# Kernel tuning notes

Hardware: AMD Instinct MI355X
Metric: run time of the kernel (lower is better)

Reference implementation:

```python
import jax, jax.numpy as jnp
import numpy as np

TEMP = 0.07
BASE_TEMP = 0.07
LOSS_WEIGHT = 0.5
BN_EPS = 1e-5

N, C_IN, H, W = 8, 512, 128, 128
FEAT_DIM = 256
N_ANCHOR, N_VIEW = 152, 26  # total_classes, n_view from max_samples=4096


def _embed(x, W1, b1, gamma, beta, W2, b2):
    # x: [N, C, H, W]; 1x1 conv -> BatchNorm (batch stats, training mode) -> ReLU -> 1x1 conv -> L2 norm over channel
    h = jnp.einsum('nchw,dc->ndhw', x, W1) + b1[None, :, None, None]
    mu = h.mean(axis=(0, 2, 3), keepdims=True)
    var = h.var(axis=(0, 2, 3), keepdims=True)
    h = (h - mu) * jax.lax.rsqrt(var + BN_EPS)
    h = h * gamma[None, :, None, None] + beta[None, :, None, None]
    h = jax.nn.relu(h)
    z = jnp.einsum('nchw,dc->ndhw', h, W2) + b2[None, :, None, None]
    nrm = jnp.sqrt(jnp.sum(z * z, axis=1, keepdims=True))
    return z / jnp.maximum(nrm, 1e-12)


def _contrastive(fS, fT, labels):
    # fS, fT: [A, V, d]; labels: [A]
    A, V, d = fS.shape
    anchor = jnp.transpose(fS, (1, 0, 2)).reshape(V * A, d)  # cat(unbind(dim=1))
    contrast = jax.lax.stop_gradient(jnp.transpose(fT, (1, 0, 2)).reshape(V * A, d))
    logits = (anchor @ contrast.T) / TEMP  # [M, M]
    logits = logits - jax.lax.stop_gradient(logits.max(axis=1, keepdims=True))
    base = (labels[:, None] == labels[None, :]).astype(logits.dtype)  # [A, A]
    mask = jnp.tile(base, (V, V))  # repeat(anchor_count, contrast_count)
    neg_mask = 1.0 - mask
    M = V * A
    mask = mask * (1.0 - jnp.eye(M, dtype=logits.dtype))  # remove self-pairs
    exp_l = jnp.exp(logits)
    neg = (exp_l * neg_mask).sum(axis=1, keepdims=True)
    log_prob = logits - jnp.log(exp_l + neg)
    mean_log_prob_pos = (mask * log_prob).sum(axis=1) / (mask.sum(axis=1) + 1e-6)
    return (-(TEMP / BASE_TEMP) * mean_log_prob_pos).mean()


def setup_inputs() -> dict:
    key = jax.random.key(0)
    ks = jax.random.split(key, 16)
    inp = {
        'preds_S': jax.random.normal(ks[0], (N, C_IN, H, W), jnp.float32),
        'preds_T': jax.random.normal(ks[1], (N, C_IN, H, W), jnp.float32),
        'sample_batch': jax.random.randint(ks[2], (N_ANCHOR,), 0, N, jnp.int32),
        'sample_idx': jax.random.randint(ks[3], (N_ANCHOR, N_VIEW), 0, H * W, jnp.int32),
        'labels_': jax.random.randint(ks[4], (N_ANCHOR,), 0, 19, jnp.int32),
    }
    def conv_params(k, cin, cout):
        k1, k2 = jax.random.split(k)
        return (jax.random.normal(k1, (cout, cin), jnp.float32) * 0.02,
                jnp.zeros((cout,), jnp.float32))
    for pfx, kw, kb in (('s', ks[5], ks[6]), ('t', ks[7], ks[8])):
        W1, b1 = conv_params(kw, C_IN, C_IN)
        W2, b2 = conv_params(kb, C_IN, FEAT_DIM)
        inp[f'{pfx}_W1'], inp[f'{pfx}_b1'] = W1, b1
        inp[f'{pfx}_gamma'] = jnp.ones((C_IN,), jnp.float32)
        inp[f'{pfx}_beta'] = jnp.zeros((C_IN,), jnp.float32)
        inp[f'{pfx}_W2'], inp[f'{pfx}_b2'] = W2, b2
    return inp


def reference(preds_S, preds_T, sample_batch, sample_idx, labels_,
              s_W1, s_b1, s_gamma, s_beta, s_W2, s_b2,
              t_W1, t_b1, t_gamma, t_beta, t_W2, t_b2):
    zS = _embed(preds_S, s_W1, s_b1, s_gamma, s_beta, s_W2, s_b2)
    zT = _embed(preds_T, t_W1, t_b1, t_gamma, t_beta, t_W2, t_b2)
    n, d, h, w = zS.shape
    fS = jnp.transpose(zS, (0, 2, 3, 1)).reshape(n, h * w, d)
    fT = jnp.transpose(zT, (0, 2, 3, 1)).reshape(n, h * w, d)
    # hard-anchor gather: [A, V, d]
    fS_ = fS[sample_batch[:, None], sample_idx]
    fT_ = fT[sample_batch[:, None], sample_idx]
    loss = _contrastive(fS_, fT_, labels_) + _contrastive(fT_, fS_, labels_)
    return LOSS_WEIGHT * loss
```

## Files before the change

kernel.cpp:

```cpp
#include <hip/hip_runtime.h>
#include <hip/hip_bf16.h>

#define A_N 152
#define V_N 26
#define M_N 3952
#define M_PAD 3968
#define CIN 512
#define FDIM 256
#define HW_SZ 16384
#define P_TOT 131072.0f
#define TEMP_INV 14.285714285714286f
#define NGRP 2048
#define LCAP 64

typedef __attribute__((ext_vector_type(8))) short bf16x8;
typedef __attribute__((ext_vector_type(4))) float f32x4;

static __device__ __forceinline__ short f2bf(float x){
  union { float f; unsigned u; } v; v.f = x;
  unsigned r = (v.u + 0x7FFFu + ((v.u >> 16) & 1u)) >> 16;
  return (short)r;
}

static __device__ __forceinline__ bf16x8 ldfrag(const short* __restrict__ base, int ld,
                                                int row, int k, int lane){
  return *(const bf16x8*)(base + (size_t)(row + (lane & 15)) * ld + k + ((lane >> 4) << 3));
}

static __device__ __forceinline__ bf16x8 ldfragP(const short* __restrict__ base,
                                                 int dtile, int ktile, int lane){
  return *(const bf16x8*)(base + ((((size_t)dtile << 4) + ktile) << 9) + (lane << 3));
}

static __device__ __forceinline__ void cvt4(short* __restrict__ lds, float4 v,
                                            int px, int tid){
  lds[(px+0)*512 + (tid ^ (((px+0)&7)<<3))] = f2bf(v.x);
  lds[(px+1)*512 + (tid ^ (((px+1)&7)<<3))] = f2bf(v.y);
  lds[(px+2)*512 + (tid ^ (((px+2)&7)<<3))] = f2bf(v.z);
  lds[(px+3)*512 + (tid ^ (((px+3)&7)<<3))] = f2bf(v.w);
}

__global__ void castw_kernel(const float* __restrict__ a0, short* __restrict__ o0,
                             const float* __restrict__ a1, short* __restrict__ o1,
                             const float* __restrict__ a2, short* __restrict__ o2,
                             const float* __restrict__ a3, short* __restrict__ o3){
  const float* a; short* o; int n;
  switch (blockIdx.y){
    case 0: a = a0; o = o0; n = CIN*CIN; break;
    case 1: a = a1; o = o1; n = CIN*CIN; break;
    case 2: a = a2; o = o2; n = FDIM*CIN; break;
    default: a = a3; o = o3; n = FDIM*CIN; break;
  }
  int i = blockIdx.x * 256 + threadIdx.x;
  if (i >= n) return;
  if (blockIdx.y < 2){
    int j  = i & 7;
    int ln = (i >> 3) & 63;
    int kt = (i >> 9) & 15;
    int dt = i >> 13;
    int row = dt * 16 + (ln & 15);
    int col = kt * 32 + ((ln >> 4) << 3) + j;
    o[i] = f2bf(a[row * CIN + col]);
  } else {
    o[i] = f2bf(a[i]);
  }
}

__global__ __launch_bounds__(64) void build_lists_kernel(
    const int* __restrict__ sb, const int* __restrict__ si,
    int* __restrict__ counts, int* __restrict__ lists){
  int m = blockIdx.x * 64 + threadIdx.x;
  if (m >= M_N) return;
  int a = m % A_N, v = m / A_N;
  int pix = si[a * V_N + v];
  int g = sb[a] * 256 + (pix >> 6);
  int slot = atomicAdd(&counts[g], 1);
  if (slot < LCAP) lists[g * LCAP + slot] = m | ((pix & 63) << 16);
}

__global__ __launch_bounds__(512, 2) void stats_kernel(
    const float* __restrict__ xS, const float* __restrict__ xT,
    const short* __restrict__ w1S, const short* __restrict__ w1T,
    float* __restrict__ stats,
    const int* __restrict__ counts, const int* __restrict__ lists,
    short* __restrict__ xsS, short* __restrict__ xsT){
  __shared__ short lds[128 * 512];
  const int t = blockIdx.y;
  const float* __restrict__ x = t ? xT : xS;
  const short* __restrict__ w1 = t ? w1T : w1S;
  float* sums = stats + t * 1024;
  short* __restrict__ xs = t ? xsT : xsS;

  const int tid  = threadIdx.x;
  const int lane = tid & 63;
  const int wave = tid >> 6;

  float rs[4] = {0.f,0.f,0.f,0.f};
  float rq[4] = {0.f,0.f,0.f,0.f};

  for (int it = 0; it < 4; ++it){
    const int T   = blockIdx.x + it * 256;
    const int n   = T >> 7;
    const int hw0 = (T & 127) << 7;
    const float* src = x + ((size_t)(n * CIN + tid)) * HW_SZ + hw0;

    const int g0 = T * 2, g1 = g0 + 1;
    int cnt0 = counts[g0]; if (cnt0 > LCAP) cnt0 = LCAP;
    int cnt1 = counts[g1]; if (cnt1 > LCAP) cnt1 = LCAP;

    #pragma unroll
    for (int ch = 0; ch < 8; ++ch){
      float4 v0 = *(const float4*)(src + ch * 16 +  0);
      float4 v1 = *(const float4*)(src + ch * 16 +  4);
      float4 v2 = *(const float4*)(src + ch * 16 +  8);
      float4 v3 = *(const float4*)(src + ch * 16 + 12);
      cvt4(lds, v0, ch * 16 +  0, tid);
      cvt4(lds, v1, ch * 16 +  4, tid);
      cvt4(lds, v2, ch * 16 +  8, tid);
      cvt4(lds, v3, ch * 16 + 12, tid);
    }
    __syncthreads();

    f32x4 acc[8][4] = {};
    {
      bf16x8 c0 = ldfragP(w1, wave*4 + 0, 0, lane);
      bf16x8 c1 = ldfragP(w1, wave*4 + 1, 0, lane);
      bf16x8 c2 = ldfragP(w1, wave*4 + 2, 0, lane);
      bf16x8 c3 = ldfragP(w1, wave*4 + 3, 0, lane);
      for (int kt = 0; kt < 16; ++kt){
        const int kn = (kt + 1) & 15;
        bf16x8 n0 = ldfragP(w1, wave*4 + 0, kn, lane);
        bf16x8 n1 = ldfragP(w1, wave*4 + 1, kn, lane);
        bf16x8 n2 = ldfragP(w1, wave*4 + 2, kn, lane);
        bf16x8 n3 = ldfragP(w1, wave*4 + 3, kn, lane);
        const int kk = kt << 5;
        #pragma unroll
        for (int pi = 0; pi < 8; ++pi){
          int px = pi*16 + (lane & 15);
          int c  = (kk + ((lane >> 4) << 3)) ^ ((px & 7) << 3);
          bf16x8 af = *(const bf16x8*)(lds + px*512 + c);
          acc[pi][0] = __builtin_amdgcn_mfma_f32_16x16x32_bf16(af, c0, acc[pi][0], 0, 0, 0);
          acc[pi][1] = __builtin_amdgcn_mfma_f32_16x16x32_bf16(af, c1, acc[pi][1], 0, 0, 0);
          acc[pi][2] = __builtin_amdgcn_mfma_f32_16x16x32_bf16(af, c2, acc[pi][2], 0, 0, 0);
          acc[pi][3] = __builtin_amdgcn_mfma_f32_16x16x32_bf16(af, c3, acc[pi][3], 0, 0, 0);
        }
        c0 = n0; c1 = n1; c2 = n2; c3 = n3;
      }
    }
    #pragma unroll
    for (int di = 0; di < 4; ++di){
      float s = 0.f, q2 = 0.f;
      #pragma unroll
      for (int pi = 0; pi < 8; ++pi)
        #pragma unroll
        for (int r = 0; r < 4; ++r){ float vv = acc[pi][di][r]; s += vv; q2 += vv*vv; }
      rs[di] += s; rq[di] += q2;
    }

    for (int s = 0; s < cnt0; ++s){
      int e = lists[g0 * LCAP + s];
      int m = e & 0xFFFF, px = e >> 16;
      xs[(size_t)m * CIN + tid] = lds[px * 512 + (tid ^ ((px & 7) << 3))];
    }
    for (int s = 0; s < cnt1; ++s){
      int e = lists[g1 * LCAP + s];
      int m = e & 0xFFFF, px = (e >> 16) + 64;
      xs[(size_t)m * CIN + tid] = lds[px * 512 + (tid ^ ((px & 7) << 3))];
    }
    __syncthreads();
  }
  #pragma unroll
  for (int di = 0; di < 4; ++di){
    float s = rs[di], q2 = rq[di];
    s  += __shfl_xor(s, 16, 64);  s  += __shfl_xor(s, 32, 64);
    q2 += __shfl_xor(q2, 16, 64); q2 += __shfl_xor(q2, 32, 64);
    if ((lane & 48) == 0){
      int d = wave * 64 + di*16 + lane;
      atomicAdd(&sums[d], s);
      atomicAdd(&sums[512 + d], q2);
    }
  }
}

__global__ __launch_bounds__(256) void conv1_kernel(
    const short* __restrict__ xsS, const short* __restrict__ xsT,
    const short* __restrict__ w1S, const short* __restrict__ w1T,
    const float* __restrict__ stats,
    const float* __restrict__ gS, const float* __restrict__ bS,
    const float* __restrict__ gT, const float* __restrict__ bT,
    short* __restrict__ hrS, short* __restrict__ hrT){
  const int t = blockIdx.z;
  const short* xs = t ? xsT : xsS;
  const short* w1 = t ? w1T : w1S;
  const float* sums  = stats + t * 1024;
  const float* gamma = t ? gT : gS;
  const float* beta  = t ? bT : bS;
  short* hr = t ? hrT : hrS;

  const int lane = threadIdx.x & 63;
  const int wave = threadIdx.x >> 6;
  const int m0 = blockIdx.x * 16;
  const int dt0 = (blockIdx.y * 4 + wave) * 4;
  const int d0  = dt0 * 16;

  f32x4 acc[4] = {};
  for (int kk = 0; kk < CIN; kk += 32){
    bf16x8 a = ldfrag(xs, CIN, m0, kk, lane);
    #pragma unroll
    for (int di = 0; di < 4; ++di){
      bf16x8 b = ldfragP(w1, dt0 + di, kk >> 5, lane);
      acc[di] = __builtin_amdgcn_mfma_f32_16x16x32_bf16(a, b, acc[di], 0, 0, 0);
    }
  }
  const float invP = 1.f / P_TOT;
  #pragma unroll
  for (int di = 0; di < 4; ++di){
    int d = d0 + di*16 + (lane & 15);
    float mu  = sums[d] * invP;
    float var = sums[512 + d] * invP - mu * mu;
    float sc  = gamma[d] * rsqrtf(var + 1e-5f);
    float sh  = beta[d] - mu * sc;
    #pragma unroll
    for (int r = 0; r < 4; ++r){
      int m = m0 + ((lane >> 4) << 2) + r;
      float v = fmaxf(acc[di][r] * sc + sh, 0.f);
      hr[(size_t)m * CIN + d] = f2bf(v);
    }
  }
}

__global__ __launch_bounds__(256) void conv2_kernel(
    const short* __restrict__ hrS, const short* __restrict__ hrT,
    const short* __restrict__ w2S, const short* __restrict__ w2T,
    const float* __restrict__ b2S, const float* __restrict__ b2T,
    short* __restrict__ fS, short* __restrict__ fT){
  __shared__ float ssum[4][16];
  const int t = blockIdx.y;
  const short* hr = t ? hrT : hrS;
  const short* w2 = t ? w2T : w2S;
  const float* b2 = t ? b2T : b2S;
  short* f = t ? fT : fS;

  const int lane = threadIdx.x & 63;
  const int wave = threadIdx.x >> 6;
  const int m0 = blockIdx.x * 16;
  const int e0 = wave * 64;

  f32x4 acc[4] = {};
  for (int kk = 0; kk < CIN; kk += 32){
    bf16x8 a = ldfrag(hr, CIN, m0, kk, lane);
    #pragma unroll
    for (int ei = 0; ei < 4; ++ei){
      bf16x8 b = ldfrag(w2, CIN, e0 + ei*16, kk, lane);
      acc[ei] = __builtin_amdgcn_mfma_f32_16x16x32_bf16(a, b, acc[ei], 0, 0, 0);
    }
  }
  float z[4][4];
  float part[4] = {0.f,0.f,0.f,0.f};
  #pragma unroll
  for (int ei = 0; ei < 4; ++ei){
    int e = e0 + ei*16 + (lane & 15);
    float bb = b2[e];
    #pragma unroll
    for (int r = 0; r < 4; ++r){
      float v = acc[ei][r] + bb;
      z[ei][r] = v;
      part[r] += v * v;
    }
  }
  #pragma unroll
  for (int r = 0; r < 4; ++r){
    float p = part[r];
    p += __shfl_xor(p, 1, 64); p += __shfl_xor(p, 2, 64);
    p += __shfl_xor(p, 4, 64); p += __shfl_xor(p, 8, 64);
    part[r] = p;
  }
  if ((lane & 15) == 0){
    #pragma unroll
    for (int r = 0; r < 4; ++r) ssum[wave][((lane >> 4) << 2) + r] = part[r];
  }
  __syncthreads();
  #pragma unroll
  for (int r = 0; r < 4; ++r){
    int mrow = ((lane >> 4) << 2) + r;
    float tot = ssum[0][mrow] + ssum[1][mrow] + ssum[2][mrow] + ssum[3][mrow];
    float sc = 1.f / fmaxf(sqrtf(tot), 1e-12f);
    #pragma unroll
    for (int ei = 0; ei < 4; ++ei){
      int e = e0 + ei*16 + (lane & 15);
      f[(size_t)(m0 + mrow) * FDIM + e] = f2bf(z[ei][r] * sc);
    }
  }
}

__global__ __launch_bounds__(256) void logits_kernel(
    const short* __restrict__ fa, const short* __restrict__ fb,
    float* __restrict__ L, float* __restrict__ LT){
  __shared__ float trl[64 * 65];
  const int tid  = threadIdx.x;
  const int lane = tid & 63;
  const int wave = tid >> 6;
  const int m0 = blockIdx.x * 64;
  const int n0 = blockIdx.y * 64;
  f32x4 acc[4] = {};
  for (int kk = 0; kk < FDIM; kk += 32){
    bf16x8 a = ldfrag(fa, FDIM, m0 + wave * 16, kk, lane);
    #pragma unroll
    for (int ni = 0; ni < 4; ++ni){
      bf16x8 b = ldfrag(fb, FDIM, n0 + ni*16, kk, lane);
      acc[ni] = __builtin_amdgcn_mfma_f32_16x16x32_bf16(a, b, acc[ni], 0, 0, 0);
    }
  }
  #pragma unroll
  for (int ni = 0; ni < 4; ++ni){
    int colL = ni*16 + (lane & 15);
    #pragma unroll
    for (int r = 0; r < 4; ++r){
      int rowL = wave*16 + ((lane >> 4) << 2) + r;
      float val = acc[ni][r] * TEMP_INV;
      L[(size_t)(m0 + rowL) * M_PAD + (n0 + colL)] = val;
      trl[colL * 65 + rowL] = val;
    }
  }
  if (LT){
    __syncthreads();
    const int rj = tid >> 2;
    const int cq = (tid & 3) << 4;
    float* dst = LT + (size_t)(n0 + rj) * M_PAD + m0 + cq;
    #pragma unroll
    for (int q = 0; q < 4; ++q){
      f32x4 tmp;
      tmp.x = trl[rj*65 + cq + q*4 + 0];
      tmp.y = trl[rj*65 + cq + q*4 + 1];
      tmp.z = trl[rj*65 + cq + q*4 + 2];
      tmp.w = trl[rj*65 + cq + q*4 + 3];
      *(f32x4*)(dst + q*4) = tmp;
    }
  }
}

__global__ __launch_bounds__(256) void loss_kernel(
    const float* __restrict__ L, const float* __restrict__ LT,
    const int* __restrict__ labels, float* __restrict__ out){
  __shared__ float row[M_N];
  __shared__ float red[4];
  const int m1 = blockIdx.x;
  const int tid = threadIdx.x;
  const int lab1 = labels[m1 % A_N];
  const float* Lr = (blockIdx.y ? LT : L) + (size_t)m1 * M_PAD;

  float mx = -3.4e38f;
  for (int j = tid; j < M_N; j += 256){ float v = Lr[j]; row[j] = v; mx = fmaxf(mx, v); }
  #pragma unroll
  for (int s = 1; s < 64; s <<= 1) mx = fmaxf(mx, __shfl_xor(mx, s, 64));
  if ((tid & 63) == 0) red[tid >> 6] = mx;
  __syncthreads();
  mx = fmaxf(fmaxf(red[0], red[1]), fmaxf(red[2], red[3]));
  __syncthreads();

  float negp = 0.f;
  for (int j = tid; j < M_N; j += 256){
    int labj = labels[j % A_N];
    float e = __expf(row[j] - mx);
    negp += (labj != lab1) ? e : 0.f;
  }
  #pragma unroll
  for (int s = 1; s < 64; s <<= 1) negp += __shfl_xor(negp, s, 64);
  if ((tid & 63) == 0) red[tid >> 6] = negp;
  __syncthreads();
  float neg = red[0] + red[1] + red[2] + red[3];
  __syncthreads();

  float ps = 0.f, pc = 0.f;
  for (int j = tid; j < M_N; j += 256){
    int labj = labels[j % A_N];
    if (labj == lab1 && j != m1){
      float l = row[j] - mx;
      ps += l - __logf(__expf(l) + neg);
      pc += 1.f;
    }
  }
  #pragma unroll
  for (int s = 1; s < 64; s <<= 1) ps += __shfl_xor(ps, s, 64);
  #pragma unroll
  for (int s = 1; s < 64; s <<= 1) pc += __shfl_xor(pc, s, 64);
  if ((tid & 63) == 0) red[tid >> 6] = ps;
  __syncthreads();
  ps = red[0] + red[1] + red[2] + red[3];
  __syncthreads();
  if ((tid & 63) == 0) red[tid >> 6] = pc;
  __syncthreads();
  if (tid == 0){
    pc = red[0] + red[1] + red[2] + red[3];
    float mlpp = ps / (pc + 1e-6f);
    atomicAdd(out, -0.5f / (float)M_N * mlpp);
  }
}

extern "C" void kernel_launch(void* const* d_in, const int* in_sizes, int n_in,
                              void* d_out, int out_size, void* d_ws, size_t ws_size,
                              hipStream_t stream){
  const float* xS     = (const float*)d_in[0];
  const float* xT     = (const float*)d_in[1];
  const int*   sb     = (const int*)d_in[2];
  const int*   si     = (const int*)d_in[3];
  const int*   labels = (const int*)d_in[4];
  const float* sW1    = (const float*)d_in[5];
  const float* sGamma = (const float*)d_in[7];
  const float* sBeta  = (const float*)d_in[8];
  const float* sW2    = (const float*)d_in[9];
  const float* sB2    = (const float*)d_in[10];
  const float* tW1    = (const float*)d_in[11];
  const float* tGamma = (const float*)d_in[13];
  const float* tBeta  = (const float*)d_in[14];
  const float* tW2    = (const float*)d_in[15];
  const float* tB2    = (const float*)d_in[16];
  float* out = (float*)d_out;

  char* ws = (char*)d_ws;
  size_t off = 0;
  auto alloc = [&](size_t bytes) -> void* {
    void* p = ws + off;
    off = (off + bytes + 255) & ~(size_t)255;
    return p;
  };
  short* w1bS = (short*)alloc((size_t)CIN * CIN * 2);
  short* w1bT = (short*)alloc((size_t)CIN * CIN * 2);
  short* w2bS = (short*)alloc((size_t)FDIM * CIN * 2);
  short* w2bT = (short*)alloc((size_t)FDIM * CIN * 2);
  float* stats = (float*)alloc(2 * 1024 * 4);
  int* counts = (int*)alloc(NGRP * 4);
  int* lists  = (int*)alloc((size_t)NGRP * LCAP * 4);
  short* xsS = (short*)alloc((size_t)M_N * CIN * 2);
  short* xsT = (short*)alloc((size_t)M_N * CIN * 2);
  short* hrS = (short*)alloc((size_t)M_N * CIN * 2);
  short* hrT = (short*)alloc((size_t)M_N * CIN * 2);
  short* fS  = (short*)alloc((size_t)M_PAD * FDIM * 2);
  short* fT  = (short*)alloc((size_t)M_PAD * FDIM * 2);
  float* L   = (float*)alloc((size_t)M_PAD * M_PAD * 4);
  float* LT  = (float*)alloc((size_t)M_PAD * M_PAD * 4);
  const bool haveLT = (off <= ws_size);

  (void)hipMemsetAsync(d_out, 0, sizeof(float), stream);
  (void)hipMemsetAsync(stats, 0, 2 * 1024 * 4, stream);
  (void)hipMemsetAsync(counts, 0, NGRP * 4, stream);
  (void)hipMemsetAsync(fS + (size_t)M_N * FDIM, 0, (size_t)(M_PAD - M_N) * FDIM * 2, stream);
  (void)hipMemsetAsync(fT + (size_t)M_N * FDIM, 0, (size_t)(M_PAD - M_N) * FDIM * 2, stream);

  castw_kernel<<<dim3((CIN*CIN + 255) / 256, 4), 256, 0, stream>>>(
      sW1, w1bS, tW1, w1bT, sW2, w2bS, tW2, w2bT);
  build_lists_kernel<<<dim3((M_N + 63) / 64), 64, 0, stream>>>(sb, si, counts, lists);

  stats_kernel<<<dim3(256, 2), 512, 0, stream>>>(xS, xT, w1bS, w1bT, stats,
                                                 counts, lists, xsS, xsT);
  conv1_kernel<<<dim3(247, 2, 2), 256, 0, stream>>>(xsS, xsT, w1bS, w1bT, stats,
                                                    sGamma, sBeta, tGamma, tBeta, hrS, hrT);
  conv2_kernel<<<dim3(247, 2), 256, 0, stream>>>(hrS, hrT, w2bS, w2bT, sB2, tB2, fS, fT);

  if (haveLT){
    logits_kernel<<<dim3(62, 62), 256, 0, stream>>>(fS, fT, L, LT);
    loss_kernel<<<dim3(M_N, 2), 256, 0, stream>>>(L, LT, labels, out);
  } else {
    logits_kernel<<<dim3(62, 62), 256, 0, stream>>>(fS, fT, L, nullptr);
    loss_kernel<<<dim3(M_N, 1), 256, 0, stream>>>(L, L, labels, out);
    logits_kernel<<<dim3(62, 62), 256, 0, stream>>>(fT, fS, L, nullptr);
    loss_kernel<<<dim3(M_N, 1), 256, 0, stream>>>(L, L, labels, out);
  }
}
```

Measured before the change: 600.3 us.

## Fuse logits GEMM and contrastive loss with online negative log-sum-exp

Replaces the separate logits and loss kernels with one fused kernel. Each block computes a 16-row strip of the similarity matrix with MFMA and keeps a running max and rescaled sum of exponentials over negative pairs. Positive-pair logits go into a shared-memory stash for a final pass. This removes the write and re-read of two large fp32 logits matrices in global memory. In exchange it adds shared-memory atomics, divergent per-element branching, and a fixed stash capacity that could drop positives if a label class were very large.

```diff
diff --git a/kernel.cpp b/kernel.cpp
--- a/kernel.cpp
+++ b/kernel.cpp
@@ -12,6 +12,7 @@
 #define TEMP_INV 14.285714285714286f
 #define NGRP 2048
 #define LCAP 64
+#define PCAP 768
 
 typedef __attribute__((ext_vector_type(8))) short bf16x8;
 typedef __attribute__((ext_vector_type(4))) float f32x4;
@@ -293,107 +294,111 @@
   }
 }
 
-__global__ __launch_bounds__(256) void logits_kernel(
-    const short* __restrict__ fa, const short* __restrict__ fb,
-    float* __restrict__ L, float* __restrict__ LT){
-  __shared__ float trl[64 * 65];
+__global__ __launch_bounds__(256) void fused_kernel(
+    const short* __restrict__ fS, const short* __restrict__ fT,
+    const int* __restrict__ labels, float* __restrict__ out){
+  __shared__ unsigned char lab[M_N];
+  __shared__ float stash[16][PCAP];
+  __shared__ int   scnt[16];
+  __shared__ float redm[4][16], reds[4][16];
+  __shared__ float fmx[16], fng[16];
+
+  const short* fa = blockIdx.y ? fT : fS;
+  const short* fb = blockIdx.y ? fS : fT;
   const int tid  = threadIdx.x;
   const int lane = tid & 63;
   const int wave = tid >> 6;
-  const int m0 = blockIdx.x * 64;
-  const int n0 = blockIdx.y * 64;
-  f32x4 acc[4] = {};
-  for (int kk = 0; kk < FDIM; kk += 32){
-    bf16x8 a = ldfrag(fa, FDIM, m0 + wave * 16, kk, lane);
+  const int m0 = blockIdx.x * 16;
+
+  for (int j = tid; j < M_N; j += 256) lab[j] = (unsigned char)labels[j % A_N];
+  if (tid < 16) scnt[tid] = 0;
+  __syncthreads();
+
+  const int rbase = (lane >> 4) << 2;
+  int labrow[4];
+  #pragma unroll
+  for (int r = 0; r < 4; ++r) labrow[r] = lab[m0 + rbase + r];
+
+  float pm[4]   = {-3.4e38f,-3.4e38f,-3.4e38f,-3.4e38f};
+  float psum[4] = {0.f,0.f,0.f,0.f};
+
+  for (int nt = wave; nt < 62; nt += 4){
+    const int n0 = nt * 64;
+    f32x4 acc[4] = {};
+    for (int kk = 0; kk < FDIM; kk += 32){
+      bf16x8 a = ldfrag(fa, FDIM, m0, kk, lane);
+      #pragma unroll
+      for (int ni = 0; ni < 4; ++ni){
+        bf16x8 b = ldfrag(fb, FDIM, n0 + ni*16, kk, lane);
+        acc[ni] = __builtin_amdgcn_mfma_f32_16x16x32_bf16(a, b, acc[ni], 0, 0, 0);
+      }
+    }
     #pragma unroll
     for (int ni = 0; ni < 4; ++ni){
-      bf16x8 b = ldfrag(fb, FDIM, n0 + ni*16, kk, lane);
-      acc[ni] = __builtin_amdgcn_mfma_f32_16x16x32_bf16(a, b, acc[ni], 0, 0, 0);
-    }
-  }
-  #pragma unroll
-  for (int ni = 0; ni < 4; ++ni){
-    int colL = ni*16 + (lane & 15);
-    #pragma unroll
-    for (int r = 0; r < 4; ++r){
-      int rowL = wave*16 + ((lane >> 4) << 2) + r;
-      float val = acc[ni][r] * TEMP_INV;
-      L[(size_t)(m0 + rowL) * M_PAD + (n0 + colL)] = val;
-      trl[colL * 65 + rowL] = val;
-    }
-  }
-  if (LT){
-    __syncthreads();
-    const int rj = tid >> 2;
-    const int cq = (tid & 3) << 4;
-    float* dst = LT + (size_t)(n0 + rj) * M_PAD + m0 + cq;
-    #pragma unroll
-    for (int q = 0; q < 4; ++q){
-      f32x4 tmp;
-      tmp.x = trl[rj*65 + cq + q*4 + 0];
-      tmp.y = trl[rj*65 + cq + q*4 + 1];
-      tmp.z = trl[rj*65 + cq + q*4 + 2];
-      tmp.w = trl[rj*65 + cq + q*4 + 3];
-      *(f32x4*)(dst + q*4) = tmp;
-    }
-  }
-}
-
-__global__ __launch_bounds__(256) void loss_kernel(
-    const float* __restrict__ L, const float* __restrict__ LT,
-    const int* __restrict__ labels, float* __restrict__ out){
-  __shared__ float row[M_N];
-  __shared__ float red[4];
-  const int m1 = blockIdx.x;
-  const int tid = threadIdx.x;
-  const int lab1 = labels[m1 % A_N];
-  const float* Lr = (blockIdx.y ? LT : L) + (size_t)m1 * M_PAD;
-
-  float mx = -3.4e38f;
-  for (int j = tid; j < M_N; j += 256){ float v = Lr[j]; row[j] = v; mx = fmaxf(mx, v); }
-  #pragma unroll
-  for (int s = 1; s < 64; s <<= 1) mx = fmaxf(mx, __shfl_xor(mx, s, 64));
-  if ((tid & 63) == 0) red[tid >> 6] = mx;
+      int col = n0 + ni*16 + (lane & 15);
+      if (col < M_N){
+        int labc = lab[col];
+        #pragma unroll
+        for (int r = 0; r < 4; ++r){
+          int rowg = m0 + rbase + r;
+          if (col == rowg) continue;
+          float l = acc[ni][r] * TEMP_INV;
+          if (labc == labrow[r]){
+            int slot = atomicAdd(&scnt[rbase + r], 1);
+            if (slot < PCAP) stash[rbase + r][slot] = l;
+          } else if (l > pm[r]){
+            psum[r] = psum[r] * __expf(pm[r] - l) + 1.f;
+            pm[r] = l;
+          } else {
+            psum[r] += __expf(l - pm[r]);
+          }
+        }
+      }
+    }
+  }
+
+  #pragma unroll
+  for (int r = 0; r < 4; ++r){
+    #pragma unroll
+    for (int s = 1; s < 16; s <<= 1){
+      float om = __shfl_xor(pm[r], s, 64);
+      float os = __shfl_xor(psum[r], s, 64);
+      float nm = fmaxf(pm[r], om);
+      psum[r] = psum[r] * __expf(pm[r] - nm) + os * __expf(om - nm);
+      pm[r] = nm;
+    }
+    if ((lane & 15) == 0){ redm[wave][rbase + r] = pm[r]; reds[wave][rbase + r] = psum[r]; }
+  }
   __syncthreads();
-  mx = fmaxf(fmaxf(red[0], red[1]), fmaxf(red[2], red[3]));
+  if (tid < 16){
+    float m = redm[0][tid], s = reds[0][tid];
+    #pragma unroll
+    for (int w = 1; w < 4; ++w){
+      float om = redm[w][tid], os = reds[w][tid];
+      float nm = fmaxf(m, om);
+      s = s * __expf(m - nm) + os * __expf(om - nm);
+      m = nm;
+    }
+    fmx[tid] = m; fng[tid] = s;
+  }
   __syncthreads();
 
-  float negp = 0.f;
-  for (int j = tid; j < M_N; j += 256){
-    int labj = labels[j % A_N];
-    float e = __expf(row[j] - mx);
-    negp += (labj != lab1) ? e : 0.f;
-  }
-  #pragma unroll
-  for (int s = 1; s < 64; s <<= 1) negp += __shfl_xor(negp, s, 64);
-  if ((tid & 63) == 0) red[tid >> 6] = negp;
-  __syncthreads();
-  float neg = red[0] + red[1] + red[2] + red[3];
-  __syncthreads();
-
-  float ps = 0.f, pc = 0.f;
-  for (int j = tid; j < M_N; j += 256){
-    int labj = labels[j % A_N];
-    if (labj == lab1 && j != m1){
-      float l = row[j] - mx;
+  {
+    const int rowl = tid >> 4;
+    const int t16  = tid & 15;
+    int cnt = scnt[rowl]; if (cnt > PCAP) cnt = PCAP;
+    const float mx = fmx[rowl], neg = fng[rowl];
+    float ps = 0.f;
+    for (int s = t16; s < cnt; s += 16){
+      float l = stash[rowl][s] - mx;
       ps += l - __logf(__expf(l) + neg);
-      pc += 1.f;
-    }
-  }
-  #pragma unroll
-  for (int s = 1; s < 64; s <<= 1) ps += __shfl_xor(ps, s, 64);
-  #pragma unroll
-  for (int s = 1; s < 64; s <<= 1) pc += __shfl_xor(pc, s, 64);
-  if ((tid & 63) == 0) red[tid >> 6] = ps;
-  __syncthreads();
-  ps = red[0] + red[1] + red[2] + red[3];
-  __syncthreads();
-  if ((tid & 63) == 0) red[tid >> 6] = pc;
-  __syncthreads();
-  if (tid == 0){
-    pc = red[0] + red[1] + red[2] + red[3];
-    float mlpp = ps / (pc + 1e-6f);
-    atomicAdd(out, -0.5f / (float)M_N * mlpp);
+    }
+    #pragma unroll
+    for (int s = 1; s < 16; s <<= 1) ps += __shfl_xor(ps, s, 64);
+    if (t16 == 0){
+      float mlpp = ps / ((float)cnt + 1e-6f);
+      atomicAdd(out, -0.5f / (float)M_N * mlpp);
+    }
   }
 }
 
@@ -437,9 +442,6 @@
   short* hrT = (short*)alloc((size_t)M_N * CIN * 2);
   short* fS  = (short*)alloc((size_t)M_PAD * FDIM * 2);
   short* fT  = (short*)alloc((size_t)M_PAD * FDIM * 2);
-  float* L   = (float*)alloc((size_t)M_PAD * M_PAD * 4);
-  float* LT  = (float*)alloc((size_t)M_PAD * M_PAD * 4);
-  const bool haveLT = (off <= ws_size);
 
   (void)hipMemsetAsync(d_out, 0, sizeof(float), stream);
   (void)hipMemsetAsync(stats, 0, 2 * 1024 * 4, stream);
@@ -457,13 +459,5 @@
                                                     sGamma, sBeta, tGamma, tBeta, hrS, hrT);
   conv2_kernel<<<dim3(247, 2), 256, 0, stream>>>(hrS, hrT, w2bS, w2bT, sB2, tB2, fS, fT);
 
-  if (haveLT){
-    logits_kernel<<<dim3(62, 62), 256, 0, stream>>>(fS, fT, L, LT);
-    loss_kernel<<<dim3(M_N, 2), 256, 0, stream>>>(L, LT, labels, out);
-  } else {
-    logits_kernel<<<dim3(62, 62), 256, 0, stream>>>(fS, fT, L, nullptr);
-    loss_kernel<<<dim3(M_N, 1), 256, 0, stream>>>(L, L, labels, out);
-    logits_kernel<<<dim3(62, 62), 256, 0, stream>>>(fT, fS, L, nullptr);
-    loss_kernel<<<dim3(M_N, 1), 256, 0, stream>>>(L, L, labels, out);
-  }
-}
+  fused_kernel<<<dim3(247, 2), 256, 0, stream>>>(fS, fT, labels, out);
+}
```

Result: faster. 537.6 us (-10.5%).
